# Performance work log

Hardware: AMD Instinct MI355X
Metric: run time of the kernel (lower is better)

## Reference

```python
import jax, jax.numpy as jnp
import numpy as np

CH = 256
HEADS = 4
RED = 8  # SE reduction on 2*CH channels


def _conv2d(x, w, pad):
    # x: [b,c,h,w], w: [o,i,kh,kw]
    return jax.lax.conv_general_dilated(
        x, w, window_strides=(1, 1), padding=[(pad, pad), (pad, pad)],
        dimension_numbers=('NCHW', 'OIHW', 'NCHW'))


def setup_inputs() -> dict:
    key = jax.random.key(0)
    ks = jax.random.split(key, 12)
    b, c, h, w = 4, CH, 64, 64
    c2 = 2 * c
    s = 0.02
    inp = {
        'color_feat': jax.random.normal(ks[0], (b, c, h, w), jnp.float32),
        'gray_feat': jax.random.normal(ks[1], (b, c, h, w), jnp.float32),
        'Wq': jax.random.normal(ks[2], (c, c), jnp.float32) * s,
        'Wk': jax.random.normal(ks[3], (c, c), jnp.float32) * s,
        'Wv': jax.random.normal(ks[4], (c, c), jnp.float32) * s,
        'Wproj': jax.random.normal(ks[5], (c, c), jnp.float32) * s,
        'ca_w1': jax.random.normal(ks[6], (c2 // RED, c2), jnp.float32) * s,
        'ca_w2': jax.random.normal(ks[7], (c2, c2 // RED), jnp.float32) * s,
        'sa_w': jax.random.normal(ks[8], (1, 2, 7, 7), jnp.float32) * s,
        'fuse_w': jax.random.normal(ks[9], (c, c2, 3, 3), jnp.float32) * s,
        'bn_gamma': jnp.ones((c,), jnp.float32),
        'bn_beta': jnp.zeros((c,), jnp.float32),
        'bn_mean': jnp.zeros((c,), jnp.float32),
        'bn_var': jnp.ones((c,), jnp.float32),
    }
    return inp


def reference(color_feat, gray_feat, Wq, Wk, Wv, Wproj, ca_w1, ca_w2,
              sa_w, fuse_w, bn_gamma, bn_beta, bn_mean, bn_var):
    b, c, h, w = color_feat.shape
    nh = HEADS
    d = c // nh
    scale = d ** -0.5

    def heads(x, W):
        # 1x1 conv then split heads: [b,c,h,w] -> [b,nh,hw,d]
        y = jnp.einsum('bchw,oc->bohw', x, W)
        return y.reshape(b, nh, d, h * w).transpose(0, 1, 3, 2)

    q = heads(color_feat, Wq)
    k = heads(gray_feat, Wk)
    v = heads(gray_feat, Wv)

    attn = jax.nn.softmax(jnp.einsum('bnid,bnjd->bnij', q, k) * scale, axis=-1)
    out = jnp.einsum('bnij,bnjd->bnid', attn, v)
    out = out.transpose(0, 1, 3, 2).reshape(b, c, h, w)
    out = jnp.einsum('bchw,oc->bohw', out, Wproj)

    cat = jnp.concatenate([out, gray_feat], axis=1)  # [b,2c,h,w]

    # Channel attention (SE with shared MLP on avg- and max-pooled vectors)
    def mlp(z):
        return jax.nn.relu(z @ ca_w1.T) @ ca_w2.T
    avg = cat.mean(axis=(2, 3))
    mx = cat.max(axis=(2, 3))
    wch = jax.nn.sigmoid(mlp(avg) + mlp(mx))[:, :, None, None]
    cat = cat * wch

    # Spatial attention: channel-mean/max -> 7x7 conv -> sigmoid gate
    sa_in = jnp.stack([cat.mean(axis=1), cat.max(axis=1)], axis=1)  # [b,2,h,w]
    wsp = jax.nn.sigmoid(_conv2d(sa_in, sa_w, pad=3))
    cat = cat * wsp

    # Fuse: 3x3 conv -> BatchNorm (inference stats) -> LeakyReLU(0.2)
    y = _conv2d(cat, fuse_w, pad=1)
    inv = bn_gamma / jnp.sqrt(bn_var + 1e-5)
    y = (y - bn_mean[None, :, None, None]) * inv[None, :, None, None] + bn_beta[None, :, None, None]
    return jnp.where(y > 0, y, 0.2 * y)
```

## Files before the change

### kernel.cpp

```cpp
#include <hip/hip_runtime.h>
#include <hip/hip_bf16.h>
#include <stdint.h>

#define HW_ 4096

typedef short bf16x8 __attribute__((ext_vector_type(8)));
typedef short short4v __attribute__((ext_vector_type(4)));
typedef short short8v __attribute__((ext_vector_type(8)));
typedef float f32x4 __attribute__((ext_vector_type(4)));
typedef float f32x16 __attribute__((ext_vector_type(16)));
typedef uint32_t u32x4 __attribute__((ext_vector_type(4)));

__device__ inline unsigned short f2bf(float x) {
  uint32_t u = __builtin_bit_cast(uint32_t, x);
  uint32_t r = ((u >> 16) & 1u) + 0x7fffu;
  return (unsigned short)((u + r) >> 16);
}
__device__ inline uint32_t cvt_pk_bf16(float lo, float hi) {
  uint32_t r;
  asm("v_cvt_pk_bf16_f32 %0, %1, %2" : "=v"(r) : "v"(lo), "v"(hi));
  return r;
}
__device__ inline float bf_lo(uint32_t u) { return __builtin_bit_cast(float, u << 16); }
__device__ inline float bf_hi(uint32_t u) { return __builtin_bit_cast(float, u & 0xffff0000u); }
__device__ inline void gld_lds16(const unsigned short* g, unsigned short* l) {
  __builtin_amdgcn_global_load_lds((const __attribute__((address_space(1))) void*)g,
                                   (__attribute__((address_space(3))) void*)l, 16, 0, 0);
}

__global__ __launch_bounds__(256) void xconv_kernel(
    const float* __restrict__ X, unsigned short* __restrict__ Y) {
  const int i = blockIdx.x * 256 + threadIdx.x;
  const int p = i & 4095;
  const int cg = (i >> 12) & 31;
  const int b = i >> 17;
  const float* src = X + ((size_t)b * 256 + cg * 8) * HW_ + p;
  float v[8];
#pragma unroll
  for (int e = 0; e < 8; ++e) v[e] = src[(size_t)e * HW_];
  uint4 o;
  o.x = cvt_pk_bf16(v[0], v[1]);
  o.y = cvt_pk_bf16(v[2], v[3]);
  o.z = cvt_pk_bf16(v[4], v[5]);
  o.w = cvt_pk_bf16(v[6], v[7]);
  *(uint4*)&Y[((size_t)(b * 32 + cg) * HW_ + p) * 8] = o;
}

__global__ __launch_bounds__(256) void prep_kernel(
    const float* __restrict__ Wq, const float* __restrict__ Wk,
    const float* __restrict__ Wv, const float* __restrict__ Wp,
    const float* __restrict__ fw,
    unsigned short* __restrict__ WqB, unsigned short* __restrict__ WkB,
    unsigned short* __restrict__ WvB, unsigned short* __restrict__ WpB,
    unsigned short* __restrict__ wt) {
  const int blk = blockIdx.x;
  if (blk < 128) {
    const int which = blk >> 5;
    const float* W = which == 0 ? Wq : which == 1 ? Wk : which == 2 ? Wv : Wp;
    unsigned short* Y = which == 0 ? WqB : which == 1 ? WkB : which == 2 ? WvB : WpB;
    const int i = (blk & 31) * 256 + threadIdx.x;
    const int o = i & 255;
    const int cg = i >> 8;
    float4 a = *(const float4*)&W[(size_t)o * 256 + cg * 8];
    float4 bq = *(const float4*)&W[(size_t)o * 256 + cg * 8 + 4];
    uint4 ov;
    ov.x = cvt_pk_bf16(a.x, a.y);
    ov.y = cvt_pk_bf16(a.z, a.w);
    ov.z = cvt_pk_bf16(bq.x, bq.y);
    ov.w = cvt_pk_bf16(bq.z, bq.w);
    *(uint4*)&Y[((size_t)cg * 256 + o) * 8] = ov;
  } else {
    const size_t i = (size_t)(blk - 128) * 256 + threadIdx.x;
    const int oc = (int)(i >> 9);
    const int ic = (int)(i & 511);
    const float* src = fw + i * 9;
#pragma unroll
    for (int tap = 0; tap < 9; ++tap)
      wt[((size_t)tap * 256 + oc) * 512 + ic] = f2bf(src[tap]);
  }
}

__global__ __launch_bounds__(256) void gemm_mfma_kernel(
    const unsigned short* __restrict__ Xbf, const unsigned short* __restrict__ Wbf,
    void* __restrict__ Yv, int mode, float oscale) {
  __shared__ unsigned short W_l[32][64][8];
  __shared__ unsigned short X_l[2][2][128][8];
  const int t = threadIdx.x;
  const int w = t >> 6;
  const int l = t & 63;
  const int n = l & 31;
  const int g32 = l >> 5;
  const int p0 = blockIdx.x * 128;
  const int o0 = blockIdx.y * 64;
  const int b = blockIdx.z;
  const int wo = w >> 1, wp = w & 1;
  const unsigned short* Xb = Xbf + (size_t)b * 32 * HW_ * 8;

  for (int i = t; i < 2048; i += 256) {
    const int ksg = i >> 6, oc = i & 63;
    gld_lds16(Wbf + ((size_t)ksg * 256 + o0 + oc) * 8, &W_l[0][0][0] + (size_t)i * 8);
  }
  {
    const int gg = t >> 7, pp = t & 127;
    gld_lds16(Xb + ((size_t)gg * HW_ + p0 + pp) * 8, &X_l[0][0][0][0] + (size_t)t * 8);
  }
  f32x16 acc[2] = {};
  int buf = 0;
  for (int ks = 0; ks < 16; ++ks) {
    asm volatile("s_waitcnt vmcnt(0)" ::: "memory");
    __syncthreads();
    if (ks < 15) {
      const int gg = t >> 7, pp = t & 127;
      gld_lds16(Xb + ((size_t)((ks + 1) * 2 + gg) * HW_ + p0 + pp) * 8,
                &X_l[buf ^ 1][0][0][0] + (size_t)t * 8);
    }
    bf16x8 af = *(const bf16x8*)&W_l[ks * 2 + g32][wo * 32 + n][0];
    bf16x8 b0 = *(const bf16x8*)&X_l[buf][g32][wp * 64 + n][0];
    bf16x8 b1 = *(const bf16x8*)&X_l[buf][g32][wp * 64 + 32 + n][0];
    acc[0] = __builtin_amdgcn_mfma_f32_32x32x16_bf16(af, b0, acc[0], 0, 0, 0);
    acc[1] = __builtin_amdgcn_mfma_f32_32x32x16_bf16(af, b1, acc[1], 0, 0, 0);
    buf ^= 1;
  }

  if (mode == 1) {
    unsigned short* Y = (unsigned short*)Yv;
    const size_t bh = (size_t)b * 4 + blockIdx.y;
#pragma unroll
    for (int pf = 0; pf < 2; ++pf) {
      const int p = p0 + wp * 64 + pf * 32 + n;
      unsigned short* dst = Y + (bh * HW_ + p) * 64 + wo * 32 + 4 * g32;
#pragma unroll
      for (int q = 0; q < 4; ++q) {
        uint2 uu;
        uu.x = cvt_pk_bf16(acc[pf][q * 4 + 0] * oscale, acc[pf][q * 4 + 1] * oscale);
        uu.y = cvt_pk_bf16(acc[pf][q * 4 + 2] * oscale, acc[pf][q * 4 + 3] * oscale);
        *(uint2*)&dst[8 * q] = uu;
      }
    }
  } else if (mode == 2) {
    unsigned short* Y = (unsigned short*)Yv;
#pragma unroll
    for (int pf = 0; pf < 2; ++pf) {
      const int p = p0 + wp * 64 + pf * 32 + n;
#pragma unroll
      for (int r = 0; r < 16; ++r) {
        const int m = (r & 3) + 8 * (r >> 2) + 4 * g32;
        Y[((size_t)b * 256 + o0 + wo * 32 + m) * HW_ + p] = f2bf(acc[pf][r]);
      }
    }
  } else {
    unsigned short* Y = (unsigned short*)Yv;
    const int cgb = (o0 + wo * 32) >> 3;
#pragma unroll
    for (int pf = 0; pf < 2; ++pf) {
      const int p = p0 + wp * 64 + pf * 32 + n;
#pragma unroll
      for (int q = 0; q < 4; ++q) {
        uint2 uu;
        uu.x = cvt_pk_bf16(acc[pf][q * 4 + 0], acc[pf][q * 4 + 1]);
        uu.y = cvt_pk_bf16(acc[pf][q * 4 + 2], acc[pf][q * 4 + 3]);
        *(uint2*)&Y[((size_t)(b * 32 + cgb + q) * HW_ + p) * 8 + 4 * g32] = uu;
      }
    }
  }
}

#define ATTN_STAGE(BUF, KP, VP)                                              \
  {                                                                          \
    gld_lds16((KP), &k_l[BUF][16 * w][0]);                                   \
    gld_lds16((KP) + (size_t)8 * 64, &k_l[BUF][16 * w + 8][0]);              \
    gld_lds16((VP), &v_l[BUF][16 * w][0]);                                   \
    gld_lds16((VP) + (size_t)8 * HW_, &v_l[BUF][16 * w + 8][0]);             \
  }

#define ATTN_COMPUTE(BUF)                                                    \
  {                                                                          \
    f32x4 accS[2][4];                                                        \
    _Pragma("unroll") for (int jt = 0; jt < 4; ++jt) {                       \
      const int jrow = jt * 16 + c;                                          \
      bf16x8 kf0 = *(const bf16x8*)&k_l[BUF][jrow][((0 + g) ^ (c & 7)) * 8]; \
      bf16x8 kf1 = *(const bf16x8*)&k_l[BUF][jrow][((4 + g) ^ (c & 7)) * 8]; \
      _Pragma("unroll") for (int qt = 0; qt < 2; ++qt) {                     \
        f32x4 s0 = __builtin_amdgcn_mfma_f32_16x16x32_bf16(kf0, qf[qt][0], zero4, 0, 0, 0); \
        accS[qt][jt] = __builtin_amdgcn_mfma_f32_16x16x32_bf16(kf1, qf[qt][1], s0, 0, 0, 0); \
      }                                                                      \
    }                                                                        \
    uint32_t pwu[2][2][4];                                                   \
    _Pragma("unroll") for (int qt = 0; qt < 2; ++qt) {                       \
      float rs = 0.f;                                                        \
      _Pragma("unroll") for (int jt = 0; jt < 4; ++jt) {                     \
        const float e0 = __builtin_amdgcn_exp2f(accS[qt][jt][0]);            \
        const float e1 = __builtin_amdgcn_exp2f(accS[qt][jt][1]);            \
        const float e2 = __builtin_amdgcn_exp2f(accS[qt][jt][2]);            \
        const float e3 = __builtin_amdgcn_exp2f(accS[qt][jt][3]);            \
        rs += (e0 + e1) + (e2 + e3);                                         \
        pwu[qt][jt >> 1][(jt & 1) * 2 + 0] = cvt_pk_bf16(e0, e1);            \
        pwu[qt][jt >> 1][(jt & 1) * 2 + 1] = cvt_pk_bf16(e2, e3);            \
      }                                                                      \
      l_r[qt] += rs;                                                         \
    }                                                                        \
    bf16x8 pf[2][2];                                                         \
    _Pragma("unroll") for (int qt = 0; qt < 2; ++qt)                         \
    _Pragma("unroll") for (int kb = 0; kb < 2; ++kb) {                       \
      u32x4 tmp = {pwu[qt][kb][0], pwu[qt][kb][1], pwu[qt][kb][2], pwu[qt][kb][3]}; \
      pf[qt][kb] = __builtin_bit_cast(bf16x8, tmp);                          \
    }                                                                        \
    _Pragma("unroll") for (int dt = 0; dt < 4; ++dt) {                       \
      const int row = dt * 16 + c;                                           \
      const int sw = c & 7;                                                  \
      _Pragma("unroll") for (int kb = 0; kb < 2; ++kb) {                     \
        union { short4v h[2]; bf16x8 v8; } vv;                               \
        vv.h[0] = *(const short4v*)&v_l[BUF][row][(((kb * 4 + 0) + (g >> 1)) ^ sw) * 8 + (g & 1) * 4]; \
        vv.h[1] = *(const short4v*)&v_l[BUF][row][(((kb * 4 + 2) + (g >> 1)) ^ sw) * 8 + (g & 1) * 4]; \
        accO[0][dt] = __builtin_amdgcn_mfma_f32_16x16x32_bf16(vv.v8, pf[0][kb], accO[0][dt], 0, 0, 0); \
        accO[1][dt] = __builtin_amdgcn_mfma_f32_16x16x32_bf16(vv.v8, pf[1][kb], accO[1][dt], 0, 0, 0); \
      }                                                                      \
    }                                                                        \
  }

__global__ __launch_bounds__(256) void attn_mfma_kernel(
    const unsigned short* __restrict__ Qb, const unsigned short* __restrict__ Kb,
    const unsigned short* __restrict__ Vb, unsigned short* __restrict__ Abf) {
  __shared__ unsigned short k_l[2][64][64];
  __shared__ unsigned short v_l[2][64][64];
  const int t = threadIdx.x;
  const int w = t >> 6;
  const int l = t & 63;
  const int g = l >> 4;
  const int c = l & 15;
  const int bid = blockIdx.x;
  const int gidx = (bid & 7) * 64 + (bid >> 3);
  const int bn = gidx >> 5;
  const int q0 = (gidx & 31) * 128 + w * 32;

  bf16x8 qf[2][2];
#pragma unroll
  for (int qt = 0; qt < 2; ++qt)
#pragma unroll
    for (int dh = 0; dh < 2; ++dh)
      qf[qt][dh] = *(const bf16x8*)&Qb[((size_t)bn * HW_ + q0 + qt * 16 + c) * 64 + dh * 32 + g * 8];

  const int srow = 16 * w + (l >> 3);
  const int schunk = (l & 7) ^ ((l >> 3) & 7);
  const unsigned short* gKp = Kb + ((size_t)bn * HW_ + srow) * 64 + schunk * 8;
  const unsigned short* gVp = Vb + ((size_t)bn * 64 + srow) * HW_ + schunk * 8;

  f32x4 accO[2][4] = {};
  float l_r[2] = {0.f, 0.f};
  const f32x4 zero4 = {0.f, 0.f, 0.f, 0.f};

  ATTN_STAGE(0, gKp, gVp);
  gKp += 4096; gVp += 64;

  for (int kt2 = 0; kt2 < 32; ++kt2) {
    asm volatile("s_waitcnt vmcnt(0)" ::: "memory");
    __syncthreads();
    ATTN_STAGE(1, gKp, gVp);
    gKp += 4096; gVp += 64;
    ATTN_COMPUTE(0)
    asm volatile("s_waitcnt vmcnt(0)" ::: "memory");
    __syncthreads();
    if (kt2 < 31) {
      ATTN_STAGE(0, gKp, gVp);
      gKp += 4096; gVp += 64;
    }
    ATTN_COMPUTE(1)
  }

  const int head = bn & 3;
  const int bb = bn >> 2;
#pragma unroll
  for (int qt = 0; qt < 2; ++qt) {
    float s = l_r[qt];
    s += __shfl_xor(s, 16);
    s += __shfl_xor(s, 32);
    const float inv = 1.0f / s;
    const int p = q0 + qt * 16 + c;
#pragma unroll
    for (int dt = 0; dt < 4; ++dt) {
      uint2 uu;
      uu.x = cvt_pk_bf16(accO[qt][dt][0] * inv, accO[qt][dt][1] * inv);
      uu.y = cvt_pk_bf16(accO[qt][dt][2] * inv, accO[qt][dt][3] * inv);
      const int cg = head * 8 + dt * 2 + (g >> 1);
      *(uint2*)&Abf[((size_t)(bb * 32 + cg) * HW_ + p) * 8 + (g & 1) * 4] = uu;
    }
  }
}

__global__ __launch_bounds__(256) void pool_kernel(
    const unsigned short* __restrict__ Pbf, const unsigned short* __restrict__ Gbf,
    float* __restrict__ pavg, float* __restrict__ pmax) {
  const int cg = blockIdx.x;
  const int b = blockIdx.y;
  const int t = threadIdx.x;
  const unsigned short* P = Pbf + (size_t)(b * 32 + cg) * HW_ * 8;
  const unsigned short* G = Gbf + (size_t)(b * 32 + cg) * HW_ * 8;
  float s[16], m[16];
#pragma unroll
  for (int i = 0; i < 16; ++i) { s[i] = 0.f; m[i] = -1e30f; }
  for (int p = t; p < HW_; p += 256) {
    uint4 a = *(const uint4*)&P[(size_t)p * 8];
    uint4 gg = *(const uint4*)&G[(size_t)p * 8];
    const uint32_t ua[4] = {a.x, a.y, a.z, a.w};
    const uint32_t ug[4] = {gg.x, gg.y, gg.z, gg.w};
#pragma unroll
    for (int q = 0; q < 4; ++q) {
      const float a0 = bf_lo(ua[q]), a1 = bf_hi(ua[q]);
      const float g0 = bf_lo(ug[q]), g1 = bf_hi(ug[q]);
      s[q * 2] += a0; s[q * 2 + 1] += a1;
      m[q * 2] = fmaxf(m[q * 2], a0); m[q * 2 + 1] = fmaxf(m[q * 2 + 1], a1);
      s[8 + q * 2] += g0; s[8 + q * 2 + 1] += g1;
      m[8 + q * 2] = fmaxf(m[8 + q * 2], g0); m[8 + q * 2 + 1] = fmaxf(m[8 + q * 2 + 1], g1);
    }
  }
#pragma unroll
  for (int i = 0; i < 16; ++i)
#pragma unroll
    for (int off = 1; off < 64; off <<= 1) {
      s[i] += __shfl_xor(s[i], off);
      m[i] = fmaxf(m[i], __shfl_xor(m[i], off));
    }
  __shared__ float red[4][32];
  const int wv = t >> 6;
  if ((t & 63) == 0) {
#pragma unroll
    for (int i = 0; i < 16; ++i) { red[wv][i] = s[i]; red[wv][16 + i] = m[i]; }
  }
  __syncthreads();
  if (t < 32) {
    const float v0 = red[0][t], v1 = red[1][t], v2 = red[2][t], v3 = red[3][t];
    if (t < 16) {
      const int ch = (t < 8) ? cg * 8 + t : 256 + cg * 8 + (t - 8);
      pavg[b * 512 + ch] = (v0 + v1 + v2 + v3) * (1.f / 4096.f);
    } else {
      const int i = t - 16;
      const int ch = (i < 8) ? cg * 8 + i : 256 + cg * 8 + (i - 8);
      pmax[b * 512 + ch] = fmaxf(fmaxf(v0, v1), fmaxf(v2, v3));
    }
  }
}

__global__ __launch_bounds__(256) void se_kernel(
    const float* __restrict__ pavg, const float* __restrict__ pmax,
    const float* __restrict__ w1, const float* __restrict__ w2,
    float* __restrict__ wch) {
  const int b = blockIdx.x;
  const int t = threadIdx.x;
  __shared__ float za[512], zm[512], hs[64];
  za[t] = pavg[b * 512 + t];
  za[256 + t] = pavg[b * 512 + 256 + t];
  zm[t] = pmax[b * 512 + t];
  zm[256 + t] = pmax[b * 512 + 256 + t];
  __syncthreads();
  if (t < 64) {
    float ha = 0.f, hm = 0.f;
    for (int c = 0; c < 512; ++c) {
      const float w = w1[t * 512 + c];
      ha += w * za[c];
      hm += w * zm[c];
    }
    hs[t] = fmaxf(ha, 0.f) + fmaxf(hm, 0.f);
  }
  __syncthreads();
  for (int o = t; o < 512; o += 256) {
    float acc = 0.f;
#pragma unroll
    for (int hh = 0; hh < 64; ++hh) acc += hs[hh] * w2[o * 64 + hh];
    wch[b * 512 + o] = 1.f / (1.f + __expf(-acc));
  }
}

__global__ __launch_bounds__(256) void sa_reduce_kernel(
    const unsigned short* __restrict__ Pbf, const unsigned short* __restrict__ Gbf,
    const float* __restrict__ wch, float* __restrict__ sa_in) {
  const int b = blockIdx.y;
  const int p = blockIdx.x * 256 + threadIdx.x;
  __shared__ float wl[512];
  wl[threadIdx.x] = wch[b * 512 + threadIdx.x];
  wl[256 + threadIdx.x] = wch[b * 512 + 256 + threadIdx.x];
  __syncthreads();
  float s = 0.f, mx = -1e30f;
#pragma unroll 4
  for (int cg = 0; cg < 32; ++cg) {
    uint4 a = *(const uint4*)&Pbf[((size_t)(b * 32 + cg) * HW_ + p) * 8];
    const uint32_t u[4] = {a.x, a.y, a.z, a.w};
#pragma unroll
    for (int q = 0; q < 4; ++q) {
      const float v0 = bf_lo(u[q]) * wl[cg * 8 + q * 2];
      const float v1 = bf_hi(u[q]) * wl[cg * 8 + q * 2 + 1];
      s += v0 + v1;
      mx = fmaxf(mx, fmaxf(v0, v1));
    }
  }
#pragma unroll 4
  for (int cg = 0; cg < 32; ++cg) {
    uint4 a = *(const uint4*)&Gbf[((size_t)(b * 32 + cg) * HW_ + p) * 8];
    const uint32_t u[4] = {a.x, a.y, a.z, a.w};
#pragma unroll
    for (int q = 0; q < 4; ++q) {
      const float v0 = bf_lo(u[q]) * wl[256 + cg * 8 + q * 2];
      const float v1 = bf_hi(u[q]) * wl[256 + cg * 8 + q * 2 + 1];
      s += v0 + v1;
      mx = fmaxf(mx, fmaxf(v0, v1));
    }
  }
  sa_in[((size_t)b * 2 + 0) * HW_ + p] = s * (1.f / 512.f);
  sa_in[((size_t)b * 2 + 1) * HW_ + p] = mx;
}

__global__ __launch_bounds__(256) void sa_conv_kernel(
    const float* __restrict__ sa_in, const float* __restrict__ sa_w,
    float* __restrict__ wsp) {
  const int b = blockIdx.y;
  const int t = threadIdx.x;
  __shared__ float pl[2][64][64];
  __shared__ float wl[98];
  for (int e = t; e < 8192; e += 256) ((float*)pl)[e] = sa_in[(size_t)b * 8192 + e];
  if (t < 98) wl[t] = sa_w[t];
  __syncthreads();
  const int pix = blockIdx.x * 256 + t;
  const int y = pix >> 6, x = pix & 63;
  float acc = 0.f;
#pragma unroll
  for (int ic = 0; ic < 2; ++ic)
#pragma unroll
    for (int ky = 0; ky < 7; ++ky) {
      const int yy = y + ky - 3;
      if (yy < 0 || yy > 63) continue;
#pragma unroll
      for (int kx = 0; kx < 7; ++kx) {
        const int xx = x + kx - 3;
        if (xx < 0 || xx > 63) continue;
        acc += pl[ic][yy][xx] * wl[ic * 49 + ky * 7 + kx];
      }
    }
  wsp[(size_t)b * HW_ + pix] = 1.f / (1.f + __expf(-acc));
}

__global__ __launch_bounds__(256) void gate_kernel(
    const unsigned short* __restrict__ Pbf, const unsigned short* __restrict__ Gbf,
    const float* __restrict__ wch, const float* __restrict__ wsp,
    unsigned short* __restrict__ catg) {
  const int yp = blockIdx.x;
  const int b = blockIdx.y;
  const int t = threadIdx.x;
  unsigned short* rowp = catg + ((size_t)b * 66 + yp) * 80 * 512;
  if (yp == 0 || yp == 65) {
    short8v z = {};
    for (int m = t; m < 5120; m += 256) *(short8v*)&rowp[m * 8] = z;
    return;
  }
  const int y = yp - 1;
  __shared__ unsigned short tile[64][512];
  __shared__ float wchl[512];
  __shared__ float wspl[64];
  for (int e = t; e < 512; e += 256) wchl[e] = wch[b * 512 + e];
  if (t < 64) wspl[t] = wsp[(size_t)b * HW_ + y * 64 + t];
  {
    short8v z = {};
    for (int m = t; m < 1024; m += 256) {
      const int col = m >> 6;
      const int xi = (col < 8) ? col : (col + 64);
      *(short8v*)&rowp[(size_t)xi * 512 + (m & 63) * 8] = z;
    }
  }
  __syncthreads();
  const int x = t & 63;
  const int cs = t >> 6;
  const float wx = wspl[x];
#pragma unroll
  for (int k = 0; k < 16; ++k) {
    const int chunk = cs * 16 + k;
    const unsigned short* src = (chunk < 32)
        ? &Pbf[((size_t)(b * 32 + chunk) * HW_ + y * 64 + x) * 8]
        : &Gbf[((size_t)(b * 32 + (chunk - 32)) * HW_ + y * 64 + x) * 8];
    uint4 a = *(const uint4*)src;
    const uint32_t u[4] = {a.x, a.y, a.z, a.w};
    uint32_t o[4];
#pragma unroll
    for (int q = 0; q < 4; ++q) {
      const float lo = bf_lo(u[q]) * wchl[chunk * 8 + q * 2] * wx;
      const float hi = bf_hi(u[q]) * wchl[chunk * 8 + q * 2 + 1] * wx;
      o[q] = cvt_pk_bf16(lo, hi);
    }
    uint4 ov = {o[0], o[1], o[2], o[3]};
    *(uint4*)&tile[x][(chunk ^ (x & 7)) * 8] = ov;
  }
  __syncthreads();
#pragma unroll
  for (int j = 0; j < 16; ++j) {
    const int xi = (t >> 6) + 4 * j;
    const int c8 = t & 63;
    uint4 v = *(const uint4*)&tile[xi][(c8 ^ (xi & 7)) * 8];
    *(uint4*)&rowp[(size_t)(xi + 8) * 512 + c8 * 8] = v;
  }
}

__global__ __launch_bounds__(256) void fuse_mfma_kernel(
    const unsigned short* __restrict__ catg, const unsigned short* __restrict__ wt,
    const float* __restrict__ bn_g, const float* __restrict__ bn_b,
    const float* __restrict__ bn_m, const float* __restrict__ bn_v,
    float* __restrict__ out) {
  __shared__ unsigned short X_l[2][6][2][80][8];
  __shared__ unsigned short W_l[2][9][2][64][8];
  __shared__ float invl[64], shl[64];
  const int t = threadIdx.x;
  const int w = t >> 6;
  const int l = t & 63;
  const int n = l & 31;
  const int g = l >> 5;
  const int i = blockIdx.x;
  const int xcd = i & 7, slot = i >> 3;
  const int ocB = slot & 3;
  const int yb = xcd + 8 * (slot >> 2);
  const int y0 = (yb & 15) * 4;
  const int o0 = ocB * 64;
  const int b = yb >> 4;

  if (t < 64) {
    const float iv = bn_g[o0 + t] * rsqrtf(bn_v[o0 + t] + 1e-5f);
    invl[t] = iv;
    shl[t] = bn_b[o0 + t] - bn_m[o0 + t] * iv;
  }

  const unsigned short* catb = catg + ((size_t)b * 66 + y0) * 80 * 512;

  auto stageX = [&](int bi, int ic0) {
    for (int wc = w; wc < 15; wc += 4) {
      const int m = wc * 64 + l;
      const int lr = m / 160;
      const int rem = m - lr * 160;
      const int half = rem / 80;
      const int xi = rem - half * 80;
      gld_lds16(catb + ((size_t)lr * 80 + xi) * 512 + ic0 + half * 8,
                &X_l[bi][0][0][0][0] + (size_t)wc * 512);
    }
  };
  auto stageW = [&](int bi, int ic0) {
    for (int wc = w; wc < 18; wc += 4) {
      const int m = wc * 64 + l;
      const int tap = m >> 7;
      const int rem = m & 127;
      const int half = rem >> 6;
      const int oc = rem & 63;
      gld_lds16(wt + ((size_t)tap * 256 + o0 + oc) * 512 + ic0 + half * 8,
                &W_l[bi][0][0][0][0] + (size_t)wc * 512);
    }
  };

  f32x16 acc[2][2] = {};

  stageX(0, 0);
  stageW(0, 0);
  int buf = 0;
  for (int ks = 0; ks < 32; ++ks) {
    asm volatile("s_waitcnt vmcnt(0)" ::: "memory");
    __syncthreads();
    if (ks < 31) {
      stageX(buf ^ 1, (ks + 1) * 16);
      stageW(buf ^ 1, (ks + 1) * 16);
    }
#pragma unroll
    for (int ky = 0; ky < 3; ++ky) {
      const int lr = w + ky;
#pragma unroll
      for (int kx = 0; kx < 3; ++kx) {
        const int tap = ky * 3 + kx;
        bf16x8 a0 = *(const bf16x8*)&W_l[buf][tap][g][n][0];
        bf16x8 a1 = *(const bf16x8*)&W_l[buf][tap][g][32 + n][0];
        bf16x8 b0 = *(const bf16x8*)&X_l[buf][lr][g][n + kx + 7][0];
        bf16x8 b1 = *(const bf16x8*)&X_l[buf][lr][g][32 + n + kx + 7][0];
        acc[0][0] = __builtin_amdgcn_mfma_f32_32x32x16_bf16(a0, b0, acc[0][0], 0, 0, 0);
        acc[0][1] = __builtin_amdgcn_mfma_f32_32x32x16_bf16(a0, b1, acc[0][1], 0, 0, 0);
        acc[1][0] = __builtin_amdgcn_mfma_f32_32x32x16_bf16(a1, b0, acc[1][0], 0, 0, 0);
        acc[1][1] = __builtin_amdgcn_mfma_f32_32x32x16_bf16(a1, b1, acc[1][1], 0, 0, 0);
      }
    }
    buf ^= 1;
  }

#pragma unroll
  for (int of = 0; of < 2; ++of)
#pragma unroll
    for (int pf = 0; pf < 2; ++pf)
#pragma unroll
      for (int r = 0; r < 16; ++r) {
        const int row = (r & 3) + 8 * (r >> 2) + 4 * g;
        const int oc = of * 32 + row;
        const float yv = acc[of][pf][r] * invl[oc] + shl[oc];
        const float ov = yv > 0.f ? yv : 0.2f * yv;
        out[((size_t)b * 256 + o0 + oc) * HW_ + (size_t)(y0 + w) * 64 + pf * 32 + n] = ov;
      }
}

extern "C" void kernel_launch(void* const* d_in, const int* in_sizes, int n_in,
                              void* d_out, int out_size, void* d_ws, size_t ws_size,
                              hipStream_t stream) {
  const float* color  = (const float*)d_in[0];
  const float* gray   = (const float*)d_in[1];
  const float* Wq     = (const float*)d_in[2];
  const float* Wk     = (const float*)d_in[3];
  const float* Wv     = (const float*)d_in[4];
  const float* Wproj  = (const float*)d_in[5];
  const float* ca_w1  = (const float*)d_in[6];
  const float* ca_w2  = (const float*)d_in[7];
  const float* sa_w   = (const float*)d_in[8];
  const float* fuse_w = (const float*)d_in[9];
  const float* bn_g   = (const float*)d_in[10];
  const float* bn_b   = (const float*)d_in[11];
  const float* bn_m   = (const float*)d_in[12];
  const float* bn_v   = (const float*)d_in[13];
  float* out = (float*)d_out;

  char* ws = (char*)d_ws;
  unsigned short* Cbf = (unsigned short*)(ws);
  unsigned short* Gbf = (unsigned short*)(ws + (8u << 20));
  unsigned short* Qbf = (unsigned short*)(ws + (16u << 20));
  unsigned short* Kbf = (unsigned short*)(ws + (24u << 20));
  unsigned short* Vbf = (unsigned short*)(ws + (32u << 20));
  unsigned short* Abf = (unsigned short*)(ws);
  unsigned short* Pbf = (unsigned short*)(ws + (16u << 20));
  unsigned short* catg = (unsigned short*)(ws + (24u << 20));
  unsigned short* WqB = (unsigned short*)(ws + (45u << 20));
  unsigned short* WkB = WqB + 65536;
  unsigned short* WvB = WkB + 65536;
  unsigned short* WpB = WvB + 65536;
  unsigned short* Wt  = (unsigned short*)(ws + (45u << 20) + (1u << 19));
  float* pavg  = (float*)(ws + (48u << 20));
  float* pmax  = pavg + 2048;
  float* wch   = pmax + 2048;
  float* sa_in = wch + 2048;
  float* wsp   = sa_in + 32768;
  (void)in_sizes; (void)n_in; (void)out_size; (void)ws_size;

  const float qscale = 0.125f * 1.44269504f;

  prep_kernel<<<dim3(640), 256, 0, stream>>>(Wq, Wk, Wv, Wproj, fuse_w,
                                             WqB, WkB, WvB, WpB, Wt);
  xconv_kernel<<<dim3(2048), 256, 0, stream>>>(color, Cbf);
  xconv_kernel<<<dim3(2048), 256, 0, stream>>>(gray, Gbf);

  dim3 g_gemm(32, 4, 4);
  gemm_mfma_kernel<<<g_gemm, 256, 0, stream>>>(Cbf, WqB, Qbf, 1, qscale);
  gemm_mfma_kernel<<<g_gemm, 256, 0, stream>>>(Gbf, WkB, Kbf, 1, 1.0f);
  gemm_mfma_kernel<<<g_gemm, 256, 0, stream>>>(Gbf, WvB, Vbf, 2, 1.0f);
  attn_mfma_kernel<<<dim3(512), 256, 0, stream>>>(Qbf, Kbf, Vbf, Abf);
  gemm_mfma_kernel<<<g_gemm, 256, 0, stream>>>(Abf, WpB, Pbf, 3, 1.0f);

  pool_kernel<<<dim3(32, 4), 256, 0, stream>>>(Pbf, Gbf, pavg, pmax);
  se_kernel<<<dim3(4), 256, 0, stream>>>(pavg, pmax, ca_w1, ca_w2, wch);
  sa_reduce_kernel<<<dim3(16, 4), 256, 0, stream>>>(Pbf, Gbf, wch, sa_in);
  sa_conv_kernel<<<dim3(16, 4), 256, 0, stream>>>(sa_in, sa_w, wsp);
  gate_kernel<<<dim3(66, 4), 256, 0, stream>>>(Pbf, Gbf, wch, wsp, catg);
  fuse_mfma_kernel<<<dim3(256), 256, 0, stream>>>(catg, Wt, bn_g, bn_b, bn_m, bn_v, out);
}
```

Before: 278.8 us.

## Split attention over keys, split pool/sa_reduce/fuse grids for more blocks

Attention is split into two key halves run as separate blocks (1024 instead of 512), writing unnormalized bf16 partial outputs and row sums that a new combine kernel adds and normalizes into the channel-grouped layout. The pool kernel is split over two spatial halves with se_kernel merging the partial sums and maxima, sa_reduce splits its channel loop across four waves with a shared-memory reduction, and the fuse conv uses 32-channel output tiles to double its grid. The aim is to fill more compute units on small grids. In exchange there is an extra launch and extra partial-result traffic, more redundant X loads in the fuse conv, and partial outputs are rounded to bf16 before being combined.

```diff
diff --git a/kernel.cpp b/kernel.cpp
--- a/kernel.cpp
+++ b/kernel.cpp
@@ -220,7 +220,8 @@
 
 __global__ __launch_bounds__(256) void attn_mfma_kernel(
     const unsigned short* __restrict__ Qb, const unsigned short* __restrict__ Kb,
-    const unsigned short* __restrict__ Vb, unsigned short* __restrict__ Abf) {
+    const unsigned short* __restrict__ Vb, unsigned short* __restrict__ Op0,
+    unsigned short* __restrict__ Op1, float* __restrict__ lpart) {
   __shared__ unsigned short k_l[2][64][64];
   __shared__ unsigned short v_l[2][64][64];
   const int t = threadIdx.x;
@@ -229,9 +230,11 @@
   const int g = l >> 4;
   const int c = l & 15;
   const int bid = blockIdx.x;
-  const int gidx = (bid & 7) * 64 + (bid >> 3);
-  const int bn = gidx >> 5;
-  const int q0 = (gidx & 31) * 128 + w * 32;
+  const int gidx = (bid & 7) * 128 + (bid >> 3);
+  const int bn = gidx >> 6;
+  const int sq = gidx & 63;
+  const int split = sq >> 5;
+  const int q0 = (sq & 31) * 128 + w * 32;
 
   bf16x8 qf[2][2];
 #pragma unroll
@@ -242,8 +245,8 @@
 
   const int srow = 16 * w + (l >> 3);
   const int schunk = (l & 7) ^ ((l >> 3) & 7);
-  const unsigned short* gKp = Kb + ((size_t)bn * HW_ + srow) * 64 + schunk * 8;
-  const unsigned short* gVp = Vb + ((size_t)bn * 64 + srow) * HW_ + schunk * 8;
+  const unsigned short* gKp = Kb + ((size_t)bn * HW_ + split * 2048 + srow) * 64 + schunk * 8;
+  const unsigned short* gVp = Vb + ((size_t)bn * 64 + srow) * HW_ + split * 2048 + schunk * 8;
 
   f32x4 accO[2][4] = {};
   float l_r[2] = {0.f, 0.f};
@@ -252,7 +255,7 @@
   ATTN_STAGE(0, gKp, gVp);
   gKp += 4096; gVp += 64;
 
-  for (int kt2 = 0; kt2 < 32; ++kt2) {
+  for (int kt2 = 0; kt2 < 16; ++kt2) {
     asm volatile("s_waitcnt vmcnt(0)" ::: "memory");
     __syncthreads();
     ATTN_STAGE(1, gKp, gVp);
@@ -260,45 +263,71 @@
     ATTN_COMPUTE(0)
     asm volatile("s_waitcnt vmcnt(0)" ::: "memory");
     __syncthreads();
-    if (kt2 < 31) {
+    if (kt2 < 15) {
       ATTN_STAGE(0, gKp, gVp);
       gKp += 4096; gVp += 64;
     }
     ATTN_COMPUTE(1)
   }
 
-  const int head = bn & 3;
-  const int bb = bn >> 2;
+  unsigned short* Op = split ? Op1 : Op0;
 #pragma unroll
   for (int qt = 0; qt < 2; ++qt) {
     float s = l_r[qt];
     s += __shfl_xor(s, 16);
     s += __shfl_xor(s, 32);
-    const float inv = 1.0f / s;
     const int p = q0 + qt * 16 + c;
+    if (l < 16) lpart[((size_t)split * 16 + bn) * HW_ + p] = s;
 #pragma unroll
     for (int dt = 0; dt < 4; ++dt) {
       uint2 uu;
-      uu.x = cvt_pk_bf16(accO[qt][dt][0] * inv, accO[qt][dt][1] * inv);
-      uu.y = cvt_pk_bf16(accO[qt][dt][2] * inv, accO[qt][dt][3] * inv);
-      const int cg = head * 8 + dt * 2 + (g >> 1);
-      *(uint2*)&Abf[((size_t)(bb * 32 + cg) * HW_ + p) * 8 + (g & 1) * 4] = uu;
-    }
-  }
+      uu.x = cvt_pk_bf16(accO[qt][dt][0], accO[qt][dt][1]);
+      uu.y = cvt_pk_bf16(accO[qt][dt][2], accO[qt][dt][3]);
+      *(uint2*)&Op[((size_t)bn * HW_ + p) * 64 + dt * 16 + g * 4] = uu;
+    }
+  }
+}
+
+__global__ __launch_bounds__(256) void attn_combine_kernel(
+    const unsigned short* __restrict__ Op0, const unsigned short* __restrict__ Op1,
+    const float* __restrict__ lpart, unsigned short* __restrict__ Abf) {
+  const int tg = blockIdx.x * 256 + threadIdx.x;
+  const int dg = tg & 7;
+  const int q = (tg >> 3) & 4095;
+  const int bn = tg >> 15;
+  const size_t oidx = ((size_t)bn * HW_ + q) * 64 + dg * 8;
+  uint4 a = *(const uint4*)&Op0[oidx];
+  uint4 b2 = *(const uint4*)&Op1[oidx];
+  const float lsum = lpart[(size_t)bn * HW_ + q] + lpart[(size_t)(16 + bn) * HW_ + q];
+  const float inv = 1.0f / lsum;
+  const uint32_t ua[4] = {a.x, a.y, a.z, a.w};
+  const uint32_t ub[4] = {b2.x, b2.y, b2.z, b2.w};
+  uint32_t o[4];
+#pragma unroll
+  for (int k = 0; k < 4; ++k) {
+    const float lo = (bf_lo(ua[k]) + bf_lo(ub[k])) * inv;
+    const float hi = (bf_hi(ua[k]) + bf_hi(ub[k])) * inv;
+    o[k] = cvt_pk_bf16(lo, hi);
+  }
+  const int head = bn & 3, bb = bn >> 2;
+  const int cg = head * 8 + dg;
+  uint4 ov = {o[0], o[1], o[2], o[3]};
+  *(uint4*)&Abf[((size_t)(bb * 32 + cg) * HW_ + q) * 8] = ov;
 }
 
 __global__ __launch_bounds__(256) void pool_kernel(
     const unsigned short* __restrict__ Pbf, const unsigned short* __restrict__ Gbf,
-    float* __restrict__ pavg, float* __restrict__ pmax) {
+    float* __restrict__ psum, float* __restrict__ pmaxH) {
   const int cg = blockIdx.x;
   const int b = blockIdx.y;
-  const int t = threadIdx.x;
-  const unsigned short* P = Pbf + (size_t)(b * 32 + cg) * HW_ * 8;
-  const unsigned short* G = Gbf + (size_t)(b * 32 + cg) * HW_ * 8;
+  const int half = blockIdx.z;
+  const int t = threadIdx.x;
+  const unsigned short* P = Pbf + ((size_t)(b * 32 + cg) * HW_ + half * 2048) * 8;
+  const unsigned short* G = Gbf + ((size_t)(b * 32 + cg) * HW_ + half * 2048) * 8;
   float s[16], m[16];
 #pragma unroll
   for (int i = 0; i < 16; ++i) { s[i] = 0.f; m[i] = -1e30f; }
-  for (int p = t; p < HW_; p += 256) {
+  for (int p = t; p < 2048; p += 256) {
     uint4 a = *(const uint4*)&P[(size_t)p * 8];
     uint4 gg = *(const uint4*)&G[(size_t)p * 8];
     const uint32_t ua[4] = {a.x, a.y, a.z, a.w};
@@ -331,26 +360,26 @@
     const float v0 = red[0][t], v1 = red[1][t], v2 = red[2][t], v3 = red[3][t];
     if (t < 16) {
       const int ch = (t < 8) ? cg * 8 + t : 256 + cg * 8 + (t - 8);
-      pavg[b * 512 + ch] = (v0 + v1 + v2 + v3) * (1.f / 4096.f);
+      psum[half * 2048 + b * 512 + ch] = v0 + v1 + v2 + v3;
     } else {
       const int i = t - 16;
       const int ch = (i < 8) ? cg * 8 + i : 256 + cg * 8 + (i - 8);
-      pmax[b * 512 + ch] = fmaxf(fmaxf(v0, v1), fmaxf(v2, v3));
+      pmaxH[half * 2048 + b * 512 + ch] = fmaxf(fmaxf(v0, v1), fmaxf(v2, v3));
     }
   }
 }
 
 __global__ __launch_bounds__(256) void se_kernel(
-    const float* __restrict__ pavg, const float* __restrict__ pmax,
+    const float* __restrict__ psum, const float* __restrict__ pmaxH,
     const float* __restrict__ w1, const float* __restrict__ w2,
     float* __restrict__ wch) {
   const int b = blockIdx.x;
   const int t = threadIdx.x;
   __shared__ float za[512], zm[512], hs[64];
-  za[t] = pavg[b * 512 + t];
-  za[256 + t] = pavg[b * 512 + 256 + t];
-  zm[t] = pmax[b * 512 + t];
-  zm[256 + t] = pmax[b * 512 + 256 + t];
+  za[t] = (psum[b * 512 + t] + psum[2048 + b * 512 + t]) * (1.f / 4096.f);
+  za[256 + t] = (psum[b * 512 + 256 + t] + psum[2048 + b * 512 + 256 + t]) * (1.f / 4096.f);
+  zm[t] = fmaxf(pmaxH[b * 512 + t], pmaxH[2048 + b * 512 + t]);
+  zm[256 + t] = fmaxf(pmaxH[b * 512 + 256 + t], pmaxH[2048 + b * 512 + 256 + t]);
   __syncthreads();
   if (t < 64) {
     float ha = 0.f, hm = 0.f;
@@ -374,38 +403,41 @@
     const unsigned short* __restrict__ Pbf, const unsigned short* __restrict__ Gbf,
     const float* __restrict__ wch, float* __restrict__ sa_in) {
   const int b = blockIdx.y;
-  const int p = blockIdx.x * 256 + threadIdx.x;
+  const int t = threadIdx.x;
+  const int px = t & 63;
+  const int sl = t >> 6;
+  const int p = blockIdx.x * 64 + px;
   __shared__ float wl[512];
-  wl[threadIdx.x] = wch[b * 512 + threadIdx.x];
-  wl[256 + threadIdx.x] = wch[b * 512 + 256 + threadIdx.x];
+  __shared__ float sred[4][64], mred[4][64];
+  wl[t] = wch[b * 512 + t];
+  wl[256 + t] = wch[b * 512 + 256 + t];
   __syncthreads();
   float s = 0.f, mx = -1e30f;
 #pragma unroll 4
-  for (int cg = 0; cg < 32; ++cg) {
-    uint4 a = *(const uint4*)&Pbf[((size_t)(b * 32 + cg) * HW_ + p) * 8];
+  for (int k = 0; k < 16; ++k) {
+    const int chunk = sl * 16 + k;
+    const unsigned short* src = (chunk < 32)
+        ? &Pbf[((size_t)(b * 32 + chunk) * HW_ + p) * 8]
+        : &Gbf[((size_t)(b * 32 + (chunk - 32)) * HW_ + p) * 8];
+    uint4 a = *(const uint4*)src;
     const uint32_t u[4] = {a.x, a.y, a.z, a.w};
 #pragma unroll
     for (int q = 0; q < 4; ++q) {
-      const float v0 = bf_lo(u[q]) * wl[cg * 8 + q * 2];
-      const float v1 = bf_hi(u[q]) * wl[cg * 8 + q * 2 + 1];
+      const float v0 = bf_lo(u[q]) * wl[chunk * 8 + q * 2];
+      const float v1 = bf_hi(u[q]) * wl[chunk * 8 + q * 2 + 1];
       s += v0 + v1;
       mx = fmaxf(mx, fmaxf(v0, v1));
     }
   }
-#pragma unroll 4
-  for (int cg = 0; cg < 32; ++cg) {
-    uint4 a = *(const uint4*)&Gbf[((size_t)(b * 32 + cg) * HW_ + p) * 8];
-    const uint32_t u[4] = {a.x, a.y, a.z, a.w};
-#pragma unroll
-    for (int q = 0; q < 4; ++q) {
-      const float v0 = bf_lo(u[q]) * wl[256 + cg * 8 + q * 2];
-      const float v1 = bf_hi(u[q]) * wl[256 + cg * 8 + q * 2 + 1];
-      s += v0 + v1;
-      mx = fmaxf(mx, fmaxf(v0, v1));
-    }
-  }
-  sa_in[((size_t)b * 2 + 0) * HW_ + p] = s * (1.f / 512.f);
-  sa_in[((size_t)b * 2 + 1) * HW_ + p] = mx;
+  sred[sl][px] = s;
+  mred[sl][px] = mx;
+  __syncthreads();
+  if (sl == 0) {
+    const float S = sred[0][px] + sred[1][px] + sred[2][px] + sred[3][px];
+    const float M = fmaxf(fmaxf(mred[0][px], mred[1][px]), fmaxf(mred[2][px], mred[3][px]));
+    sa_in[((size_t)b * 2 + 0) * HW_ + p] = S * (1.f / 512.f);
+    sa_in[((size_t)b * 2 + 1) * HW_ + p] = M;
+  }
 }
 
 __global__ __launch_bounds__(256) void sa_conv_kernel(
@@ -502,8 +534,8 @@
     const float* __restrict__ bn_m, const float* __restrict__ bn_v,
     float* __restrict__ out) {
   __shared__ unsigned short X_l[2][6][2][80][8];
-  __shared__ unsigned short W_l[2][9][2][64][8];
-  __shared__ float invl[64], shl[64];
+  __shared__ unsigned short W_l[2][9][2][32][8];
+  __shared__ float invl[32], shl[32];
   const int t = threadIdx.x;
   const int w = t >> 6;
   const int l = t & 63;
@@ -511,13 +543,13 @@
   const int g = l >> 5;
   const int i = blockIdx.x;
   const int xcd = i & 7, slot = i >> 3;
-  const int ocB = slot & 3;
-  const int yb = xcd + 8 * (slot >> 2);
+  const int ocB = slot & 7;
+  const int yb = xcd + 8 * (slot >> 3);
   const int y0 = (yb & 15) * 4;
-  const int o0 = ocB * 64;
+  const int o0 = ocB * 32;
   const int b = yb >> 4;
 
-  if (t < 64) {
+  if (t < 32) {
     const float iv = bn_g[o0 + t] * rsqrtf(bn_v[o0 + t] + 1e-5f);
     invl[t] = iv;
     shl[t] = bn_b[o0 + t] - bn_m[o0 + t] * iv;
@@ -537,18 +569,18 @@
     }
   };
   auto stageW = [&](int bi, int ic0) {
-    for (int wc = w; wc < 18; wc += 4) {
+    for (int wc = w; wc < 9; wc += 4) {
       const int m = wc * 64 + l;
-      const int tap = m >> 7;
-      const int rem = m & 127;
-      const int half = rem >> 6;
-      const int oc = rem & 63;
+      const int tap = m >> 6;
+      const int rem = m & 63;
+      const int half = rem >> 5;
+      const int oc = rem & 31;
       gld_lds16(wt + ((size_t)tap * 256 + o0 + oc) * 512 + ic0 + half * 8,
                 &W_l[bi][0][0][0][0] + (size_t)wc * 512);
     }
   };
 
-  f32x16 acc[2][2] = {};
+  f32x16 acc[2] = {};
 
   stageX(0, 0);
   stageW(0, 0);
@@ -567,30 +599,24 @@
       for (int kx = 0; kx < 3; ++kx) {
         const int tap = ky * 3 + kx;
         bf16x8 a0 = *(const bf16x8*)&W_l[buf][tap][g][n][0];
-        bf16x8 a1 = *(const bf16x8*)&W_l[buf][tap][g][32 + n][0];
         bf16x8 b0 = *(const bf16x8*)&X_l[buf][lr][g][n + kx + 7][0];
         bf16x8 b1 = *(const bf16x8*)&X_l[buf][lr][g][32 + n + kx + 7][0];
-        acc[0][0] = __builtin_amdgcn_mfma_f32_32x32x16_bf16(a0, b0, acc[0][0], 0, 0, 0);
-        acc[0][1] = __builtin_amdgcn_mfma_f32_32x32x16_bf16(a0, b1, acc[0][1], 0, 0, 0);
-        acc[1][0] = __builtin_amdgcn_mfma_f32_32x32x16_bf16(a1, b0, acc[1][0], 0, 0, 0);
-        acc[1][1] = __builtin_amdgcn_mfma_f32_32x32x16_bf16(a1, b1, acc[1][1], 0, 0, 0);
+        acc[0] = __builtin_amdgcn_mfma_f32_32x32x16_bf16(a0, b0, acc[0], 0, 0, 0);
+        acc[1] = __builtin_amdgcn_mfma_f32_32x32x16_bf16(a0, b1, acc[1], 0, 0, 0);
       }
     }
     buf ^= 1;
   }
 
 #pragma unroll
-  for (int of = 0; of < 2; ++of)
-#pragma unroll
-    for (int pf = 0; pf < 2; ++pf)
-#pragma unroll
-      for (int r = 0; r < 16; ++r) {
-        const int row = (r & 3) + 8 * (r >> 2) + 4 * g;
-        const int oc = of * 32 + row;
-        const float yv = acc[of][pf][r] * invl[oc] + shl[oc];
-        const float ov = yv > 0.f ? yv : 0.2f * yv;
-        out[((size_t)b * 256 + o0 + oc) * HW_ + (size_t)(y0 + w) * 64 + pf * 32 + n] = ov;
-      }
+  for (int pf = 0; pf < 2; ++pf)
+#pragma unroll
+    for (int r = 0; r < 16; ++r) {
+      const int row = (r & 3) + 8 * (r >> 2) + 4 * g;
+      const float yv = acc[pf][r] * invl[row] + shl[row];
+      const float ov = yv > 0.f ? yv : 0.2f * yv;
+      out[((size_t)b * 256 + o0 + row) * HW_ + (size_t)(y0 + w) * 64 + pf * 32 + n] = ov;
+    }
 }
 
 extern "C" void kernel_launch(void* const* d_in, const int* in_sizes, int n_in,
@@ -618,17 +644,20 @@
   unsigned short* Qbf = (unsigned short*)(ws + (16u << 20));
   unsigned short* Kbf = (unsigned short*)(ws + (24u << 20));
   unsigned short* Vbf = (unsigned short*)(ws + (32u << 20));
-  unsigned short* Abf = (unsigned short*)(ws);
-  unsigned short* Pbf = (unsigned short*)(ws + (16u << 20));
+  unsigned short* Abf = (unsigned short*)(ws + (16u << 20));
+  unsigned short* Pbf = (unsigned short*)(ws);
+  unsigned short* Op0 = (unsigned short*)(ws);
+  unsigned short* Op1 = (unsigned short*)(ws + (48u << 20));
+  float* lpart        = (float*)(ws + (56u << 20));
   unsigned short* catg = (unsigned short*)(ws + (24u << 20));
   unsigned short* WqB = (unsigned short*)(ws + (45u << 20));
   unsigned short* WkB = WqB + 65536;
   unsigned short* WvB = WkB + 65536;
   unsigned short* WpB = WvB + 65536;
   unsigned short* Wt  = (unsigned short*)(ws + (45u << 20) + (1u << 19));
-  float* pavg  = (float*)(ws + (48u << 20));
-  float* pmax  = pavg + 2048;
-  float* wch   = pmax + 2048;
+  float* psum  = (float*)(ws + (57u << 20));
+  float* pmaxH = psum + 4096;
+  float* wch   = pmaxH + 4096;
   float* sa_in = wch + 2048;
   float* wsp   = sa_in + 32768;
   (void)in_sizes; (void)n_in; (void)out_size; (void)ws_size;
@@ -644,13 +673,14 @@
   gemm_mfma_kernel<<<g_gemm, 256, 0, stream>>>(Cbf, WqB, Qbf, 1, qscale);
   gemm_mfma_kernel<<<g_gemm, 256, 0, stream>>>(Gbf, WkB, Kbf, 1, 1.0f);
   gemm_mfma_kernel<<<g_gemm, 256, 0, stream>>>(Gbf, WvB, Vbf, 2, 1.0f);
-  attn_mfma_kernel<<<dim3(512), 256, 0, stream>>>(Qbf, Kbf, Vbf, Abf);
+  attn_mfma_kernel<<<dim3(1024), 256, 0, stream>>>(Qbf, Kbf, Vbf, Op0, Op1, lpart);
+  attn_combine_kernel<<<dim3(2048), 256, 0, stream>>>(Op0, Op1, lpart, Abf);
   gemm_mfma_kernel<<<g_gemm, 256, 0, stream>>>(Abf, WpB, Pbf, 3, 1.0f);
 
-  pool_kernel<<<dim3(32, 4), 256, 0, stream>>>(Pbf, Gbf, pavg, pmax);
-  se_kernel<<<dim3(4), 256, 0, stream>>>(pavg, pmax, ca_w1, ca_w2, wch);
-  sa_reduce_kernel<<<dim3(16, 4), 256, 0, stream>>>(Pbf, Gbf, wch, sa_in);
+  pool_kernel<<<dim3(32, 4, 2), 256, 0, stream>>>(Pbf, Gbf, psum, pmaxH);
+  se_kernel<<<dim3(4), 256, 0, stream>>>(psum, pmaxH, ca_w1, ca_w2, wch);
+  sa_reduce_kernel<<<dim3(64, 4), 256, 0, stream>>>(Pbf, Gbf, wch, sa_in);
   sa_conv_kernel<<<dim3(16, 4), 256, 0, stream>>>(sa_in, sa_w, wsp);
   gate_kernel<<<dim3(66, 4), 256, 0, stream>>>(Pbf, Gbf, wch, wsp, catg);
-  fuse_mfma_kernel<<<dim3(256), 256, 0, stream>>>(catg, Wt, bn_g, bn_b, bn_m, bn_v, out);
-}
+  fuse_mfma_kernel<<<dim3(512), 256, 0, stream>>>(catg, Wt, bn_g, bn_b, bn_m, bn_v, out);
+}
```

After: 267.5 us. 1.04x faster.
